# Performance work log

Measured on AMD Instinct MI355X. Metric: run time of the kernel, lower is better.

The kernel has to match this reference:

```python
import jax, jax.numpy as jnp
import numpy as np

B, N, DIM = 2, 1024, 512
HEADS, DIM_HEAD = 8, 64
HIDDEN = HEADS * DIM_HEAD
TIME_DIM = 512
BIAS_DIM = 16
EPS = 1e-5


def setup_inputs() -> dict:
    key = jax.random.key(0)
    ks = jax.random.split(key, 12)
    inp = {
        "x": jax.random.normal(ks[0], (B, N, DIM), jnp.float32),
        "residx": jnp.broadcast_to(jnp.arange(N, dtype=jnp.float32), (B, N)),
        "time": jax.random.normal(ks[1], (B, 1, TIME_DIM), jnp.float32),
        "attn_bias": jax.random.normal(ks[2], (B, BIAS_DIM, N, N), jnp.float32),
        "seq_mask": jnp.ones((B, N), jnp.float32),
        # params
        "gamma": jnp.ones((DIM,), jnp.float32),
        "Wt": jax.random.normal(ks[3], (2 * DIM, TIME_DIM), jnp.float32) * 0.02,
        "bt": jax.random.normal(ks[4], (2 * DIM,), jnp.float32) * 0.02,
        "Wb": jax.random.normal(ks[5], (HEADS, BIAS_DIM), jnp.float32) * 0.1,
        "bb": jax.random.normal(ks[6], (HEADS,), jnp.float32) * 0.1,
        "Wq": jax.random.normal(ks[7], (HIDDEN, DIM), jnp.float32) * (DIM ** -0.5),
        "Wkv": jax.random.normal(ks[8], (2 * HIDDEN, DIM), jnp.float32) * (DIM ** -0.5),
        "Wo": jax.random.normal(ks[9], (DIM, HIDDEN), jnp.float32) * (HIDDEN ** -0.5),
    }
    return inp


def _layer_norm(x, gamma):
    mu = jnp.mean(x, axis=-1, keepdims=True)
    var = jnp.var(x, axis=-1, keepdims=True)
    return (x - mu) * jax.lax.rsqrt(var + EPS) * gamma  # beta buffer is zeros


def reference(x, residx, time, attn_bias, seq_mask, gamma, Wt, bt, Wb, bb, Wq, Wkv, Wo):
    h, d = HEADS, DIM_HEAD
    b, n, _ = x.shape
    xn = _layer_norm(x, gamma)
    # time conditioning: SiLU -> Linear -> chunk into scale/shift
    t = jax.nn.silu(time) @ Wt.T + bt  # [B,1,2*dim]
    scale, shift = jnp.split(t, 2, axis=-1)
    xn = xn * (scale + 1.0) + shift
    xn = xn * seq_mask[..., None]
    # projections
    q = (xn @ Wq.T).reshape(b, n, h, d).transpose(0, 2, 1, 3)  # b h n d
    kv = xn @ Wkv.T
    k_, v_ = jnp.split(kv, 2, axis=-1)
    k = k_.reshape(b, n, h, d).transpose(0, 2, 1, 3)
    v = v_.reshape(b, n, h, d).transpose(0, 2, 1, 3)
    q = q * (d ** -0.5)
    sim = jnp.einsum('bhid,bhjd->bhij', q, k)
    # attn bias projection: b a i j -> linear over a -> b h i j
    bias = jnp.einsum('baij,ha->bhij', attn_bias, Wb) + bb[None, :, None, None]
    sim = sim + bias
    # mask
    attn_mask = seq_mask[:, None, :, None] * seq_mask[:, None, None, :]  # b 1 i j
    sim = sim - (1.0 - attn_mask) * 1e6
    attn = jax.nn.softmax(sim, axis=-1)
    out = jnp.einsum('bhij,bhjd->bhid', attn, v)
    out = out.transpose(0, 2, 1, 3).reshape(b, n, h * d)
    out = out @ Wo.T
    out = out * seq_mask[..., None]
    return out
```

## Files before the change

kernel.cpp:

```cpp
#include <hip/hip_runtime.h>
#include <cstdint>
#include <cstddef>

typedef __bf16 bf16x8 __attribute__((ext_vector_type(8)));
typedef float f32x4 __attribute__((ext_vector_type(4)));
typedef unsigned short u16;
typedef unsigned short u16x8 __attribute__((ext_vector_type(8)));

__device__ __forceinline__ u16 f2b(float f) {
    union { float f; uint32_t u; } v; v.f = f;
    uint32_t r = v.u + 0x7fffu + ((v.u >> 16) & 1u);
    return (u16)(r >> 16);
}
__device__ __forceinline__ float b2f(u16 h) {
    union { uint32_t u; float f; } v; v.u = ((uint32_t)h) << 16; return v.f;
}

__global__ __launch_bounds__(256) void prep_kernel(
    const float* __restrict__ Wq, const float* __restrict__ Wkv, const float* __restrict__ Wo,
    const float* __restrict__ timep, const float* __restrict__ Wt, const float* __restrict__ bt,
    u16* __restrict__ wqkv, u16* __restrict__ wo, float* __restrict__ tbuf)
{
    __shared__ float st[512];
    int bx = blockIdx.x, tid = threadIdx.x;
    if (bx < 1024) {
        int i = bx * 256 + tid;
        float4 v; u16* dp;
        if (i < 65536)      { v = ((const float4*)Wq)[i];            dp = wqkv + (size_t)i * 4; }
        else if (i < 196608){ int k = i - 65536;  v = ((const float4*)Wkv)[k]; dp = wqkv + 262144 + (size_t)k * 4; }
        else                { int k = i - 196608; v = ((const float4*)Wo)[k];  dp = wo + (size_t)k * 4; }
        ushort4 o;
        o.x = f2b(v.x); o.y = f2b(v.y); o.z = f2b(v.z); o.w = f2b(v.w);
        *(ushort4*)dp = o;
    } else {
        int bx2 = bx - 1024;
        int b = bx2 >> 2, ch = bx2 & 3;
        for (int k = tid; k < 512; k += 256) {
            float v = timep[b * 512 + k];
            st[k] = v / (1.f + __expf(-v));
        }
        __syncthreads();
        int o = ch * 256 + tid;
        const float4* wrow = (const float4*)(Wt + (size_t)o * 512);
        float acc = bt[o];
        #pragma unroll 4
        for (int k4 = 0; k4 < 128; k4++) {
            float4 w = wrow[k4];
            acc += st[k4*4+0]*w.x + st[k4*4+1]*w.y + st[k4*4+2]*w.z + st[k4*4+3]*w.w;
        }
        tbuf[b * 1024 + o] = acc;
    }
}

__global__ __launch_bounds__(64) void ln_cond_kernel(
    const float* __restrict__ x, const float* __restrict__ gamma,
    const float* __restrict__ tbuf, const float* __restrict__ seq_mask,
    u16* __restrict__ xn)
{
    int m = blockIdx.x;
    int b = m >> 10;
    int lane = threadIdx.x;
    const float* xr = x + (size_t)m * 512;
    int c0 = lane * 8;
    float4 v0 = *(const float4*)(xr + c0);
    float4 v1 = *(const float4*)(xr + c0 + 4);
    float xv[8] = {v0.x, v0.y, v0.z, v0.w, v1.x, v1.y, v1.z, v1.w};
    float s = 0.f, ss = 0.f;
    #pragma unroll
    for (int e = 0; e < 8; e++) { s += xv[e]; ss += xv[e]*xv[e]; }
    #pragma unroll
    for (int off = 1; off < 64; off <<= 1) {
        s  += __shfl_xor(s, off);
        ss += __shfl_xor(ss, off);
    }
    float mu = s * (1.f/512.f);
    float var = ss * (1.f/512.f) - mu*mu;
    float rs = rsqrtf(var + 1e-5f);
    float mk = seq_mask[m];
    u16x8 ov;
    #pragma unroll
    for (int e = 0; e < 8; e++) {
        int c = c0 + e;
        float sc = tbuf[b*1024 + c] + 1.f;
        float sh = tbuf[b*1024 + 512 + c];
        float val = ((xv[e] - mu) * rs * gamma[c] * sc + sh) * mk;
        ov[e] = f2b(val);
    }
    *(u16x8*)&xn[(size_t)m * 512 + c0] = ov;
}

__global__ __launch_bounds__(256) void qkv_bias_kernel(
    const float* __restrict__ ab, const float* __restrict__ Wb, const float* __restrict__ bbv,
    const u16* __restrict__ xn, const u16* __restrict__ wqkv,
    u16* __restrict__ bias_t, u16* __restrict__ qb, u16* __restrict__ kb, u16* __restrict__ vT)
{
    __shared__ u16 As[128][40];
    __shared__ u16 Bs[128][40];
    __shared__ float wbs[128];
    __shared__ float bbs[8];
    const int tid = threadIdx.x;
    const int bx = blockIdx.x;
    if (bx < 512) {
        if (tid < 128) wbs[tid] = Wb[tid];
        if (tid < 8) bbs[tid] = bbv[tid];
        __syncthreads();
        int t = bx * 256 + tid;
        int b = t >> 16;
        int rem = t & 65535;
        int iq = rem >> 8, jq = rem & 255;
        int i = iq * 4, j = jq * 4;
        f32x4 acc[8][4];
        #pragma unroll
        for (int h = 0; h < 8; h++)
            #pragma unroll
            for (int r = 0; r < 4; r++) {
                float bv = bbs[h];
                acc[h][r][0] = bv; acc[h][r][1] = bv; acc[h][r][2] = bv; acc[h][r][3] = bv;
            }
        for (int a = 0; a < 16; a++) {
            f32x4 v[4];
            #pragma unroll
            for (int r = 0; r < 4; r++) {
                const f32x4* src = (const f32x4*)&ab[(((size_t)(b*16 + a)) << 20) + ((size_t)(i + r) << 10) + j];
                v[r] = __builtin_nontemporal_load(src);
            }
            #pragma unroll
            for (int h = 0; h < 8; h++) {
                float w = wbs[h*16 + a];
                #pragma unroll
                for (int r = 0; r < 4; r++) acc[h][r] += w * v[r];
            }
        }
        int it32 = iq >> 3, jt = jq >> 4;
        int isub = (iq >> 2) & 1, g = iq & 3;
        int li0 = (jq & 3) * 4, fj = (jq >> 2) & 3;
        #pragma unroll
        for (int h = 0; h < 8; h++) {
            size_t base = ((((size_t)(b*8 + h))*32 + it32)*16 + jt)*2048 + fj*4;
            #pragma unroll
            for (int c = 0; c < 4; c++) {
                ushort4 o;
                o.x = f2b(acc[h][0][c]); o.y = f2b(acc[h][1][c]);
                o.z = f2b(acc[h][2][c]); o.w = f2b(acc[h][3][c]);
                *(ushort4*)&bias_t[base + (size_t)(isub*64 + g*16 + li0 + c)*16] = o;
            }
        }
    } else {
        int v = bx - 512;
        const int m0 = (v & 15) * 128, n0 = (v >> 4) * 128;
        const int lane = tid & 63, wid = tid >> 6;
        const int wr = wid >> 1, wc = wid & 1;
        const int li = lane & 15, g = lane >> 4;
        f32x4 acc[4][4] = {};
        const int srow = tid >> 2, scol = (tid & 3) * 8;
        for (int k0 = 0; k0 < 512; k0 += 32) {
            *(bf16x8*)&As[srow][scol]      = *(const bf16x8*)&xn[(size_t)(m0+srow)*512 + k0 + scol];
            *(bf16x8*)&As[srow+64][scol]   = *(const bf16x8*)&xn[(size_t)(m0+srow+64)*512 + k0 + scol];
            *(bf16x8*)&Bs[srow][scol]      = *(const bf16x8*)&wqkv[(size_t)(n0+srow)*512 + k0 + scol];
            *(bf16x8*)&Bs[srow+64][scol]   = *(const bf16x8*)&wqkv[(size_t)(n0+srow+64)*512 + k0 + scol];
            __syncthreads();
            bf16x8 a[4], bf[4];
            #pragma unroll
            for (int mi = 0; mi < 4; mi++) a[mi]  = *(const bf16x8*)&As[wr*64 + mi*16 + li][g*8];
            #pragma unroll
            for (int nj = 0; nj < 4; nj++) bf[nj] = *(const bf16x8*)&Bs[wc*64 + nj*16 + li][g*8];
            #pragma unroll
            for (int mi = 0; mi < 4; mi++)
                #pragma unroll
                for (int nj = 0; nj < 4; nj++)
                    acc[mi][nj] = __builtin_amdgcn_mfma_f32_16x16x32_bf16(a[mi], bf[nj], acc[mi][nj], 0, 0, 0);
            __syncthreads();
        }
        #pragma unroll
        for (int mi = 0; mi < 4; mi++)
            #pragma unroll
            for (int nj = 0; nj < 4; nj++) {
                int o = n0 + wc*64 + nj*16 + li;
                int m_base = m0 + wr*64 + mi*16 + g*4;
                if (o < 1024) {
                    #pragma unroll
                    for (int r = 0; r < 4; r++) {
                        int m = m_base + r;
                        int b = m >> 10, n = m & 1023;
                        float vv = acc[mi][nj][r];
                        if (o < 512) {
                            qb[((size_t)(b*8 + (o>>6))*1024 + n)*64 + (o&63)] = f2b(vv * 0.125f);
                        } else {
                            int oo = o - 512;
                            kb[((size_t)(b*8 + (oo>>6))*1024 + n)*64 + (oo&63)] = f2b(vv);
                        }
                    }
                } else {
                    int oo = o - 1024;
                    int b = m_base >> 10, n = m_base & 1023;
                    ushort4 ov;
                    ov.x = f2b(acc[mi][nj][0]); ov.y = f2b(acc[mi][nj][1]);
                    ov.z = f2b(acc[mi][nj][2]); ov.w = f2b(acc[mi][nj][3]);
                    *(ushort4*)&vT[((size_t)(b*8 + (oo>>6))*64 + (oo&63))*1024 + n] = ov;
                }
            }
    }
}

__global__ __launch_bounds__(256) void attn_kernel(
    const u16* __restrict__ qb, const u16* __restrict__ kb, const u16* __restrict__ vT,
    const u16* __restrict__ bias_t, const float* __restrict__ seq_mask,
    float* __restrict__ Om, float* __restrict__ ml)
{
    __shared__ u16 Ks[2][4096];
    __shared__ u16 Vs[2][4096];
    __shared__ u16 Ps[4][1024];
    __shared__ float mjs[512];
    int tid = threadIdx.x;
    int lane = tid & 63, w = tid >> 6;
    int li = lane & 15, g = lane >> 4;
    int it = blockIdx.x, h = blockIdx.y;
    int bz = blockIdx.z;
    int b = bz >> 1, jh = bz & 1;
    int bh = b*8 + h;
    int i0 = it * 64;
    int jt0 = jh * 8;
    const u16* qp = qb + ((size_t)bh*1024 + i0) * 64;
    const u16* kp = kb + (size_t)bh*65536 + (size_t)jt0*4096;
    const u16* vp = vT + (size_t)bh*65536;
    const u16* bp = bias_t + (((size_t)(bh*32 + it*2 + (w>>1)))*16 + jt0)*2048 + ((w&1)*64 + lane)*16;

    if (tid < 128) ((float4*)mjs)[tid] = ((const float4*)(seq_mask + b*1024 + jh*512))[tid];

    bf16x8 aq0 = *(const bf16x8*)&qp[(w*16 + li)*64 + g*8];
    bf16x8 aq1 = *(const bf16x8*)&qp[(w*16 + li)*64 + 32 + g*8];

    const int sli = tid & 15, sg = (tid >> 4) & 3, sf = tid >> 6;
    const int kslot0 = (sf*128 + sg*16 + sli) * 8;
    bf16x8 kr0, kr1, vr0, vr1, bfA_c, bfB_c, bfA_n, bfB_n;
    #define LOADT(jx) do { \
        kr0 = *(const bf16x8*)&kp[(size_t)(jx)*4096 + (sf*16 + sli)*64 + sg*8]; \
        kr1 = *(const bf16x8*)&kp[(size_t)(jx)*4096 + (sf*16 + sli)*64 + 32 + sg*8]; \
        vr0 = *(const bf16x8*)&vp[(size_t)(sf*16 + sli)*1024 + (jt0+(jx))*64 + sg*8]; \
        vr1 = *(const bf16x8*)&vp[(size_t)(sf*16 + sli)*1024 + (jt0+(jx))*64 + 32 + sg*8]; \
        bfA_n = *(const bf16x8*)&bp[(size_t)(jx)*2048]; \
        bfB_n = *(const bf16x8*)&bp[(size_t)(jx)*2048 + 8]; \
    } while (0)
    #define STORET(buf_) do { \
        *(bf16x8*)&Ks[buf_][kslot0]       = kr0; \
        *(bf16x8*)&Ks[buf_][kslot0 + 512] = kr1; \
        *(bf16x8*)&Vs[buf_][kslot0]       = vr0; \
        *(bf16x8*)&Vs[buf_][kslot0 + 512] = vr1; \
    } while (0)

    f32x4 oacc[4] = {};
    float m_run[4], l_run[4], mi[4];
    #pragma unroll
    for (int r = 0; r < 4; r++) {
        m_run[r] = -3e38f; l_run[r] = 0.f;
        mi[r] = seq_mask[b*1024 + i0 + w*16 + g*4 + r];
    }

    LOADT(0); STORET(0); bfA_c = bfA_n; bfB_c = bfB_n;
    __syncthreads();

    for (int jtt = 0; jtt < 8; jtt++) {
        int cur = jtt & 1;
        if (jtt < 7) LOADT(jtt + 1);
        f32x4 s[4] = {};
        #pragma unroll
        for (int fj = 0; fj < 4; fj++) {
            bf16x8 bk0 = *(const bf16x8*)&Ks[cur][(fj*128 + g*16 + li)*8];
            bf16x8 bk1 = *(const bf16x8*)&Ks[cur][(fj*128 + g*16 + li)*8 + 512];
            s[fj] = __builtin_amdgcn_mfma_f32_16x16x32_bf16(aq0, bk0, s[fj], 0, 0, 0);
            s[fj] = __builtin_amdgcn_mfma_f32_16x16x32_bf16(aq1, bk1, s[fj], 0, 0, 0);
        }
        float pmax[4] = {-3e38f, -3e38f, -3e38f, -3e38f};
        #pragma unroll
        for (int fj = 0; fj < 4; fj++) {
            float mj = mjs[jtt*64 + fj*16 + li];
            #pragma unroll
            for (int r = 0; r < 4; r++) {
                float bvl = (fj < 2) ? b2f(((u16x8)bfA_c)[(fj&1)*4 + r]) : b2f(((u16x8)bfB_c)[(fj&1)*4 + r]);
                float sv = s[fj][r] + bvl;
                sv -= (1.f - mi[r]*mj) * 1e6f;
                s[fj][r] = sv;
                pmax[r] = fmaxf(pmax[r], sv);
            }
        }
        #pragma unroll
        for (int r = 0; r < 4; r++)
            #pragma unroll
            for (int off = 1; off < 16; off <<= 1)
                pmax[r] = fmaxf(pmax[r], __shfl_xor(pmax[r], off));
        float alpha[4], psum[4] = {0.f, 0.f, 0.f, 0.f}, mnew[4];
        #pragma unroll
        for (int r = 0; r < 4; r++) {
            mnew[r] = fmaxf(m_run[r], pmax[r]);
            alpha[r] = __expf(m_run[r] - mnew[r]);
            m_run[r] = mnew[r];
        }
        #pragma unroll
        for (int fj = 0; fj < 4; fj++)
            #pragma unroll
            for (int r = 0; r < 4; r++) {
                float p = __expf(s[fj][r] - mnew[r]);
                s[fj][r] = p;
                psum[r] += p;
            }
        #pragma unroll
        for (int r = 0; r < 4; r++) {
            #pragma unroll
            for (int off = 1; off < 16; off <<= 1) psum[r] += __shfl_xor(psum[r], off);
            l_run[r] = l_run[r]*alpha[r] + psum[r];
        }
        #pragma unroll
        for (int fj = 0; fj < 4; fj++) {
            int ph2 = fj >> 1;
            int pg = (fj*2 + (li >> 3)) & 3;
            int pin = li & 7;
            #pragma unroll
            for (int r = 0; r < 4; r++)
                Ps[w][(ph2*64 + pg*16 + g*4 + r)*8 + pin] = f2b(s[fj][r]);
        }
        #pragma unroll
        for (int fd = 0; fd < 4; fd++)
            #pragma unroll
            for (int r = 0; r < 4; r++)
                oacc[fd][r] *= alpha[r];
        bf16x8 ap0 = *(const bf16x8*)&Ps[w][(g*16 + li)*8];
        bf16x8 ap1 = *(const bf16x8*)&Ps[w][(g*16 + li)*8 + 512];
        #pragma unroll
        for (int fd = 0; fd < 4; fd++) {
            bf16x8 bv0 = *(const bf16x8*)&Vs[cur][(fd*128 + g*16 + li)*8];
            bf16x8 bv1 = *(const bf16x8*)&Vs[cur][(fd*128 + g*16 + li)*8 + 512];
            oacc[fd] = __builtin_amdgcn_mfma_f32_16x16x32_bf16(ap0, bv0, oacc[fd], 0, 0, 0);
            oacc[fd] = __builtin_amdgcn_mfma_f32_16x16x32_bf16(ap1, bv1, oacc[fd], 0, 0, 0);
        }
        if (jtt < 7) { STORET(cur ^ 1); bfA_c = bfA_n; bfB_c = bfB_n; }
        __syncthreads();
    }
    size_t pbase = ((size_t)(bh*16 + it)*2 + jh) * 4096;
    #pragma unroll
    for (int fd = 0; fd < 4; fd++)
        #pragma unroll
        for (int r = 0; r < 4; r++)
            Om[pbase + (size_t)(w*16 + g*4 + r)*64 + fd*16 + li] = oacc[fd][r];
    if (li == 0) {
        #pragma unroll
        for (int r = 0; r < 4; r++) {
            size_t mb = ((size_t)(bh*16 + it)*2 + jh) * 128 + (w*16 + g*4 + r)*2;
            ml[mb] = m_run[r]; ml[mb + 1] = l_run[r];
        }
    }
    #undef LOADT
    #undef STORET
}

__global__ __launch_bounds__(256) void merge_kernel(
    const float* __restrict__ Om, const float* __restrict__ ml, u16* __restrict__ aout)
{
    int blk = blockIdx.x;
    int bh = blk >> 4, it = blk & 15;
    int b = bh >> 3, h = bh & 7;
    int tid = threadIdx.x;
    int row = tid >> 2, dc = (tid & 3) * 16;
    size_t p0 = ((size_t)blk*2 + 0)*4096 + (size_t)row*64 + dc;
    size_t p1 = ((size_t)blk*2 + 1)*4096 + (size_t)row*64 + dc;
    size_t m0i = ((size_t)blk*2 + 0)*128 + row*2;
    size_t m1i = ((size_t)blk*2 + 1)*128 + row*2;
    float m0 = ml[m0i], l0 = ml[m0i + 1];
    float m1 = ml[m1i], l1 = ml[m1i + 1];
    float mm = fmaxf(m0, m1);
    float e0 = __expf(m0 - mm), e1 = __expf(m1 - mm);
    float linv = 1.f / (l0*e0 + l1*e1);
    int i = it*64 + row;
    u16* op = &aout[((size_t)(b*1024 + i))*512 + h*64 + dc];
    #pragma unroll
    for (int c4 = 0; c4 < 4; c4++) {
        f32x4 v0 = *(const f32x4*)&Om[p0 + c4*4];
        f32x4 v1 = *(const f32x4*)&Om[p1 + c4*4];
        ushort4 o;
        o.x = f2b((v0[0]*e0 + v1[0]*e1)*linv);
        o.y = f2b((v0[1]*e0 + v1[1]*e1)*linv);
        o.z = f2b((v0[2]*e0 + v1[2]*e1)*linv);
        o.w = f2b((v0[3]*e0 + v1[3]*e1)*linv);
        *(ushort4*)&op[c4*4] = o;
    }
}

__global__ __launch_bounds__(256) void out_gemm_kernel(
    const u16* __restrict__ aout, const u16* __restrict__ wo,
    const float* __restrict__ seq_mask, float* __restrict__ out)
{
    __shared__ u16 As[64][40];
    __shared__ u16 Bs[64][40];
    const int tid = threadIdx.x;
    const int lane = tid & 63, wid = tid >> 6;
    const int wr = wid >> 1, wc = wid & 1;
    const int li = lane & 15, g = lane >> 4;
    const int m0 = blockIdx.x * 64, n0 = blockIdx.y * 64;

    f32x4 acc[2][2] = {};
    const int lrow = tid >> 2, lcol = (tid & 3) * 8;
    for (int k0 = 0; k0 < 512; k0 += 32) {
        *(bf16x8*)&As[lrow][lcol] = *(const bf16x8*)&aout[(size_t)(m0+lrow)*512 + k0 + lcol];
        *(bf16x8*)&Bs[lrow][lcol] = *(const bf16x8*)&wo[(size_t)(n0+lrow)*512 + k0 + lcol];
        __syncthreads();
        bf16x8 a[2], bf[2];
        #pragma unroll
        for (int fi = 0; fi < 2; fi++) a[fi]  = *(const bf16x8*)&As[wr*32 + fi*16 + li][g*8];
        #pragma unroll
        for (int fj = 0; fj < 2; fj++) bf[fj] = *(const bf16x8*)&Bs[wc*32 + fj*16 + li][g*8];
        #pragma unroll
        for (int fi = 0; fi < 2; fi++)
            #pragma unroll
            for (int fj = 0; fj < 2; fj++)
                acc[fi][fj] = __builtin_amdgcn_mfma_f32_16x16x32_bf16(a[fi], bf[fj], acc[fi][fj], 0, 0, 0);
        __syncthreads();
    }
    #pragma unroll
    for (int fi = 0; fi < 2; fi++)
        #pragma unroll
        for (int fj = 0; fj < 2; fj++)
            #pragma unroll
            for (int r = 0; r < 4; r++) {
                int m = m0 + wr*32 + fi*16 + g*4 + r;
                int o = n0 + wc*32 + fj*16 + li;
                out[(size_t)m*512 + o] = acc[fi][fj][r] * seq_mask[m];
            }
}

extern "C" void kernel_launch(void* const* d_in, const int* in_sizes, int n_in,
                              void* d_out, int out_size, void* d_ws, size_t ws_size,
                              hipStream_t stream) {
    const float* x         = (const float*)d_in[0];
    const float* timep     = (const float*)d_in[2];
    const float* attn_bias = (const float*)d_in[3];
    const float* seq_mask  = (const float*)d_in[4];
    const float* gamma     = (const float*)d_in[5];
    const float* Wt        = (const float*)d_in[6];
    const float* bt        = (const float*)d_in[7];
    const float* Wb        = (const float*)d_in[8];
    const float* bb        = (const float*)d_in[9];
    const float* Wq        = (const float*)d_in[10];
    const float* Wkv       = (const float*)d_in[11];
    const float* Wo        = (const float*)d_in[12];
    float* out = (float*)d_out;

    char* ws = (char*)d_ws;
    size_t off = 0;
    auto alloc = [&](size_t bytes) { char* p = ws + off; off += (bytes + 255) & ~(size_t)255; return p; };
    float* tbuf  = (float*)alloc(2 * 1024 * 4);
    u16* xn      = (u16*)alloc((size_t)2048 * 512 * 2);
    u16* wqkv    = (u16*)alloc((size_t)1536 * 512 * 2);
    u16* wo      = (u16*)alloc((size_t)512 * 512 * 2);
    u16* qb      = (u16*)alloc((size_t)2 * 8 * 1024 * 64 * 2);
    u16* kb      = (u16*)alloc((size_t)2 * 8 * 1024 * 64 * 2);
    u16* vT      = (u16*)alloc((size_t)2 * 8 * 64 * 1024 * 2);
    u16* bias_t  = (u16*)alloc((size_t)2 * 8 * 1024 * 1024 * 2);
    u16* aout    = (u16*)alloc((size_t)2048 * 512 * 2);
    float* Om    = (float*)alloc((size_t)256 * 2 * 4096 * 4);
    float* ml    = (float*)alloc((size_t)256 * 2 * 128 * 4);
    (void)ws_size;

    prep_kernel<<<1032, 256, 0, stream>>>(Wq, Wkv, Wo, timep, Wt, bt, wqkv, wo, tbuf);
    ln_cond_kernel<<<2048, 64, 0, stream>>>(x, gamma, tbuf, seq_mask, xn);
    qkv_bias_kernel<<<704, 256, 0, stream>>>(attn_bias, Wb, bb, xn, wqkv, bias_t, qb, kb, vT);
    attn_kernel<<<dim3(16, 8, 4), 256, 0, stream>>>(qb, kb, vT, bias_t, seq_mask, Om, ml);
    merge_kernel<<<256, 256, 0, stream>>>(Om, ml, aout);
    out_gemm_kernel<<<dim3(32, 8), 256, 0, stream>>>(aout, wo, seq_mask, out);
}
```

Before: 101.4 us.

## Split attn-bias projection into 4x more threads with reorganized bias tile layout

The attention-bias projection now gives each thread one row and four strided columns instead of a 4x4 tile, which quadruples the block count for that part of the fused kernel from 512 to 2048. Each thread batches eight bias-channel loads before the accumulation, and the packed bf16 bias tile layout changes so each thread can write one ushort4 per head. The attention kernel's unpacking of the bias fragments is changed to match the new layout. This should raise memory-level parallelism and occupancy on the bandwidth-bound 134 MB bias read. In exchange, the 16-byte vector loads become scalar loads at 64-byte stride, and the nontemporal hint is dropped.

```diff
diff --git a/kernel.cpp b/kernel.cpp
--- a/kernel.cpp
+++ b/kernel.cpp
@@ -100,53 +100,52 @@
     __shared__ float bbs[8];
     const int tid = threadIdx.x;
     const int bx = blockIdx.x;
-    if (bx < 512) {
+    if (bx < 2048) {
         if (tid < 128) wbs[tid] = Wb[tid];
         if (tid < 8) bbs[tid] = bbv[tid];
         __syncthreads();
         int t = bx * 256 + tid;
-        int b = t >> 16;
-        int rem = t & 65535;
-        int iq = rem >> 8, jq = rem & 255;
-        int i = iq * 4, j = jq * 4;
-        f32x4 acc[8][4];
-        #pragma unroll
-        for (int h = 0; h < 8; h++)
-            #pragma unroll
-            for (int r = 0; r < 4; r++) {
-                float bv = bbs[h];
-                acc[h][r][0] = bv; acc[h][r][1] = bv; acc[h][r][2] = bv; acc[h][r][3] = bv;
+        int b = t >> 18;
+        int rem = t & 262143;
+        int r  = rem & 3;
+        int li = (rem >> 2) & 15;
+        int jt = (rem >> 6) & 15;
+        int i4 = rem >> 10;
+        int i  = i4*4 + r;
+        int it32 = i4 >> 3, isub = (i4 >> 2) & 1, g = i4 & 3;
+        int slot = isub*64 + g*16 + li;
+        int voff = (i << 10) + jt*64 + li;
+
+        float acc[8][4] = {};
+        #pragma unroll
+        for (int a8 = 0; a8 < 2; a8++) {
+            float v[8][4];
+            #pragma unroll
+            for (int aa = 0; aa < 8; aa++) {
+                const float* pp = ab + (((size_t)(b*16 + a8*8 + aa)) << 20) + voff;
+                #pragma unroll
+                for (int fj = 0; fj < 4; fj++) v[aa][fj] = pp[fj*16];
             }
-        for (int a = 0; a < 16; a++) {
-            f32x4 v[4];
-            #pragma unroll
-            for (int r = 0; r < 4; r++) {
-                const f32x4* src = (const f32x4*)&ab[(((size_t)(b*16 + a)) << 20) + ((size_t)(i + r) << 10) + j];
-                v[r] = __builtin_nontemporal_load(src);
-            }
-            #pragma unroll
-            for (int h = 0; h < 8; h++) {
-                float w = wbs[h*16 + a];
+            #pragma unroll
+            for (int aa = 0; aa < 8; aa++)
                 #pragma unroll
-                for (int r = 0; r < 4; r++) acc[h][r] += w * v[r];
-            }
-        }
-        int it32 = iq >> 3, jt = jq >> 4;
-        int isub = (iq >> 2) & 1, g = iq & 3;
-        int li0 = (jq & 3) * 4, fj = (jq >> 2) & 3;
+                for (int h = 0; h < 8; h++) {
+                    float w = wbs[h*16 + a8*8 + aa];
+                    #pragma unroll
+                    for (int fj = 0; fj < 4; fj++) acc[h][fj] += w * v[aa][fj];
+                }
+        }
         #pragma unroll
         for (int h = 0; h < 8; h++) {
-            size_t base = ((((size_t)(b*8 + h))*32 + it32)*16 + jt)*2048 + fj*4;
-            #pragma unroll
-            for (int c = 0; c < 4; c++) {
-                ushort4 o;
-                o.x = f2b(acc[h][0][c]); o.y = f2b(acc[h][1][c]);
-                o.z = f2b(acc[h][2][c]); o.w = f2b(acc[h][3][c]);
-                *(ushort4*)&bias_t[base + (size_t)(isub*64 + g*16 + li0 + c)*16] = o;
-            }
+            float bv = bbs[h];
+            ushort4 o;
+            o.x = f2b(acc[h][0] + bv); o.y = f2b(acc[h][1] + bv);
+            o.z = f2b(acc[h][2] + bv); o.w = f2b(acc[h][3] + bv);
+            size_t addr = ((((size_t)(b*8 + h))*32 + it32)*16 + jt)*2048 + slot*16 + r*4;
+            *(ushort4*)&bias_t[addr] = o;
         }
     } else {
-        int v = bx - 512;
+        int v = bx - 2048;
         const int m0 = (v & 15) * 128, n0 = (v >> 4) * 128;
         const int lane = tid & 63, wid = tid >> 6;
         const int wr = wid >> 1, wc = wid & 1;
@@ -276,7 +275,7 @@
             float mj = mjs[jtt*64 + fj*16 + li];
             #pragma unroll
             for (int r = 0; r < 4; r++) {
-                float bvl = (fj < 2) ? b2f(((u16x8)bfA_c)[(fj&1)*4 + r]) : b2f(((u16x8)bfB_c)[(fj&1)*4 + r]);
+                float bvl = (r < 2) ? b2f(((u16x8)bfA_c)[r*4 + fj]) : b2f(((u16x8)bfB_c)[(r-2)*4 + fj]);
                 float sv = s[fj][r] + bvl;
                 sv -= (1.f - mi[r]*mj) * 1e6f;
                 s[fj][r] = sv;
@@ -461,7 +460,7 @@
 
     prep_kernel<<<1032, 256, 0, stream>>>(Wq, Wkv, Wo, timep, Wt, bt, wqkv, wo, tbuf);
     ln_cond_kernel<<<2048, 64, 0, stream>>>(x, gamma, tbuf, seq_mask, xn);
-    qkv_bias_kernel<<<704, 256, 0, stream>>>(attn_bias, Wb, bb, xn, wqkv, bias_t, qb, kb, vT);
+    qkv_bias_kernel<<<2240, 256, 0, stream>>>(attn_bias, Wb, bb, xn, wqkv, bias_t, qb, kb, vT);
     attn_kernel<<<dim3(16, 8, 4), 256, 0, stream>>>(qb, kb, vT, bias_t, seq_mask, Om, ml);
     merge_kernel<<<256, 256, 0, stream>>>(Om, ml, aout);
     out_gemm_kernel<<<dim3(32, 8), 256, 0, stream>>>(aout, wo, seq_mask, out);
```

Result: faster. 95.58 us (-5.7%).
